# Optimization experiments

Hardware: AMD Instinct MI355X
Metric: run time of the kernel (lower is better)

## Reference

```python
import jax, jax.numpy as jnp
import numpy as np

B, S, T, D = 32, 8, 128, 768   # batch, num_sentences, seq_len, embedding_dim
A, L = 8, 8                    # num_args, arg_length


def _extract(sentence_embeddings, sentence_ids, token_ids):
    """Vectorized form of extract_embeddings_from_ids.

    For each (b, s, a): average, over nonzero token ids l, the embedding at the
    sentence position whose id equals token_ids[b,s,a,l]. token_id == 0 is skipped.
    sentence_ids are unique per sentence, so each id matches exactly one position
    (the only case where the original loop yields shape [B,S,A,D]).
    """
    valid = token_ids != 0                                            # [B,S,A,L]
    # match[b,s,a,l,t] = token matches sentence position t (and token is nonzero)
    match = (token_ids[..., None] == sentence_ids[:, :, None, None, :]) & valid[..., None]
    # gather matched embeddings per token: [B,S,A,L,D]
    gathered = jnp.einsum('bsalt,bstd->bsald', match.astype(sentence_embeddings.dtype),
                          sentence_embeddings)
    n_valid = jnp.maximum(valid.sum(-1), 1).astype(sentence_embeddings.dtype)  # [B,S,A]
    return gathered.sum(axis=3) / n_valid[..., None]                  # [B,S,A,D]


def setup_inputs() -> dict:
    key = jax.random.key(0)
    k_emb, k_p, k_a0, k_a1 = jax.random.split(key, 4)
    sentence_embeddings = jax.random.normal(k_emb, (B, S, T, D), dtype=jnp.float32)
    # unique token ids 1..T per sentence (0 is reserved as padding/skip)
    sentence_ids = jnp.broadcast_to(jnp.arange(1, T + 1, dtype=jnp.int64), (B, S, T))
    predicate_ids = jax.random.randint(k_p, (B, S, A, L), 0, T, dtype=jnp.int64)
    arg0_ids = jax.random.randint(k_a0, (B, S, A, L), 0, T, dtype=jnp.int64)
    arg1_ids = jax.random.randint(k_a1, (B, S, A, L), 0, T, dtype=jnp.int64)
    return {
        'sentence_embeddings': sentence_embeddings,
        'sentence_ids': sentence_ids,
        'predicate_ids': predicate_ids,
        'arg0_ids': arg0_ids,
        'arg1_ids': arg1_ids,
    }


def reference(sentence_embeddings, sentence_ids, predicate_ids, arg0_ids, arg1_ids):
    sentence_average_embeddings = sentence_embeddings.mean(axis=2)     # [B,S,D]
    predicate_embeddings = _extract(sentence_embeddings, sentence_ids, predicate_ids)
    arg0_embeddings = _extract(sentence_embeddings, sentence_ids, arg0_ids)
    arg1_embeddings = _extract(sentence_embeddings, sentence_ids, arg1_ids)
    return (sentence_average_embeddings, predicate_embeddings,
            arg0_embeddings, arg1_embeddings)
```

## Files before the change

### kernel.cpp

```cpp
#include <hip/hip_runtime.h>

namespace {
constexpr int B_ = 32, S_ = 8, T_ = 128, D_ = 768, A_ = 8, L_ = 8;
constexpr int BS = B_ * S_;
constexpr int MEAN_ELEMS = BS * D_;
constexpr int EXT_ELEMS  = BS * A_ * D_;
constexpr int MEAN_BLOCKS = BS * (D_ / 2) / 256;
constexpr int EXT_BLOCKS  = 3 * BS * A_;

__global__ void __launch_bounds__(256) srl_kernel(
    const float* __restrict__ emb,
    const int* __restrict__ sids,
    const int* __restrict__ pred,
    const int* __restrict__ arg0,
    const int* __restrict__ arg1,
    float* __restrict__ out)
{
    const int blk = blockIdx.x;
    const int tid = threadIdx.x;

    if (blk < MEAN_BLOCKS) {
        int idx = blk * 256 + tid;
        int d2  = idx % (D_ / 2);
        int bs  = idx / (D_ / 2);
        const float2* p = reinterpret_cast<const float2*>(emb)
                          + (size_t)bs * T_ * (D_ / 2) + d2;
        float sx = 0.f, sy = 0.f;
        #pragma unroll 8
        for (int t = 0; t < T_; ++t) {
            float2 v = p[(size_t)t * (D_ / 2)];
            sx += v.x; sy += v.y;
        }
        float2 r; r.x = sx * (1.0f / T_); r.y = sy * (1.0f / T_);
        reinterpret_cast<float2*>(out)[(size_t)bs * (D_ / 2) + d2] = r;
        return;
    }

    int eblk = blk - MEAN_BLOCKS;
    int e    = eblk / (BS * A_);
    int rem  = eblk % (BS * A_);
    int bs   = rem / A_;
    int a    = rem % A_;
    const int* tokp = (e == 0 ? pred : (e == 1 ? arg0 : arg1))
                      + (size_t)(bs * A_ + a) * L_;

    __shared__ int toks[L_];
    __shared__ int pos[L_];
    if (tid < L_) { toks[tid] = tokp[tid]; pos[tid] = -1; }
    __syncthreads();
    if (tid < T_) {
        int id = sids[(size_t)bs * T_ + tid];
        #pragma unroll
        for (int l = 0; l < L_; ++l)
            if (toks[l] != 0 && id == toks[l]) pos[l] = tid;
    }
    __syncthreads();

    int n = 0;
    #pragma unroll
    for (int l = 0; l < L_; ++l) n += (toks[l] != 0);
    float inv = 1.0f / (float)(n < 1 ? 1 : n);

    const float* base = emb + (size_t)bs * T_ * D_;
    float a0 = 0.f, a1 = 0.f, a2 = 0.f;
    #pragma unroll
    for (int l = 0; l < L_; ++l) {
        int p = pos[l];
        if (p >= 0) {
            const float* row = base + (size_t)p * D_;
            a0 += row[tid];
            a1 += row[tid + 256];
            a2 += row[tid + 512];
        }
    }
    float* o = out + MEAN_ELEMS + (size_t)e * EXT_ELEMS + (size_t)(bs * A_ + a) * D_;
    o[tid]       = a0 * inv;
    o[tid + 256] = a1 * inv;
    o[tid + 512] = a2 * inv;
}
}

extern "C" void kernel_launch(void* const* d_in, const int* in_sizes, int n_in,
                              void* d_out, int out_size, void* d_ws, size_t ws_size,
                              hipStream_t stream) {
    const float* emb  = (const float*)d_in[0];
    const int*   sids = (const int*)d_in[1];
    const int*   pred = (const int*)d_in[2];
    const int*   arg0 = (const int*)d_in[3];
    const int*   arg1 = (const int*)d_in[4];
    float* out = (float*)d_out;

    dim3 grid(MEAN_BLOCKS + EXT_BLOCKS);
    srl_kernel<<<grid, 256, 0, stream>>>(emb, sids, pred, arg0, arg1, out);
}
```

Baseline: 41.77 us.

## Fuse mean and gather into one block per sentence with per-token count weights

Replaces the separate mean blocks and per-(extraction,arg) gather blocks with a single block per sentence. Each block streams the sentence embeddings once, accumulating the mean and all 24 extraction outputs using packed per-position match counts held in shared memory, with double-buffered register loads. This avoids re-reading embedding rows across many small blocks, but it launches only 256 blocks of 384 threads, which lowers parallelism, and it raises register pressure from 24 float2 accumulators.

Measured after the change: 58.53 us. +40.1%, slower.

```diff
diff --git a/kernel.cpp b/kernel.cpp
--- a/kernel.cpp
+++ b/kernel.cpp
@@ -5,10 +5,11 @@
 constexpr int BS = B_ * S_;
 constexpr int MEAN_ELEMS = BS * D_;
 constexpr int EXT_ELEMS  = BS * A_ * D_;
-constexpr int MEAN_BLOCKS = BS * (D_ / 2) / 256;
-constexpr int EXT_BLOCKS  = 3 * BS * A_;
+constexpr int NO   = 3 * A_;
+constexpr int NTOK = NO * L_;
+constexpr int NTHR = 384;
 
-__global__ void __launch_bounds__(256) srl_kernel(
+__global__ void __launch_bounds__(NTHR, 1) srl_fused(
     const float* __restrict__ emb,
     const int* __restrict__ sids,
     const int* __restrict__ pred,
@@ -16,67 +17,107 @@
     const int* __restrict__ arg1,
     float* __restrict__ out)
 {
-    const int blk = blockIdx.x;
+    const int bs  = blockIdx.x;
     const int tid = threadIdx.x;
 
-    if (blk < MEAN_BLOCKS) {
-        int idx = blk * 256 + tid;
-        int d2  = idx % (D_ / 2);
-        int bs  = idx / (D_ / 2);
-        const float2* p = reinterpret_cast<const float2*>(emb)
-                          + (size_t)bs * T_ * (D_ / 2) + d2;
-        float sx = 0.f, sy = 0.f;
-        #pragma unroll 8
-        for (int t = 0; t < T_; ++t) {
-            float2 v = p[(size_t)t * (D_ / 2)];
-            sx += v.x; sy += v.y;
-        }
-        float2 r; r.x = sx * (1.0f / T_); r.y = sy * (1.0f / T_);
-        reinterpret_cast<float2*>(out)[(size_t)bs * (D_ / 2) + d2] = r;
-        return;
+    __shared__ int toks[NTOK];
+    __shared__ unsigned cnt[NO][T_];
+    __shared__ __attribute__((aligned(16))) unsigned packed[T_][8];
+    __shared__ float invs[NO];
+
+    if (tid < NTOK) {
+        int e = tid >> 6;
+        const int* p = (e == 0) ? pred : ((e == 1) ? arg0 : arg1);
+        toks[tid] = p[(size_t)bs * 64 + (tid & 63)];
     }
+    for (int i = tid; i < NO * T_; i += NTHR) ((unsigned*)cnt)[i] = 0u;
+    __syncthreads();
 
-    int eblk = blk - MEAN_BLOCKS;
-    int e    = eblk / (BS * A_);
-    int rem  = eblk % (BS * A_);
-    int bs   = rem / A_;
-    int a    = rem % A_;
-    const int* tokp = (e == 0 ? pred : (e == 1 ? arg0 : arg1))
-                      + (size_t)(bs * A_ + a) * L_;
-
-    __shared__ int toks[L_];
-    __shared__ int pos[L_];
-    if (tid < L_) { toks[tid] = tokp[tid]; pos[tid] = -1; }
-    __syncthreads();
     if (tid < T_) {
         int id = sids[(size_t)bs * T_ + tid];
+        if (id != 0) {
+            for (int i = 0; i < NTOK; ++i)
+                if (toks[i] == id) atomicAdd(&cnt[i >> 3][tid], 1u);
+        }
+    } else if (tid >= 320 && tid < 320 + NO) {
+        int o = tid - 320, n = 0;
         #pragma unroll
-        for (int l = 0; l < L_; ++l)
-            if (toks[l] != 0 && id == toks[l]) pos[l] = tid;
+        for (int l = 0; l < L_; ++l) n += (toks[o * L_ + l] != 0);
+        invs[o] = 1.0f / (float)(n < 1 ? 1 : n);
     }
     __syncthreads();
 
-    int n = 0;
+    if (tid < T_) {
+        #pragma unroll
+        for (int j = 0; j < 6; ++j) {
+            unsigned v = 0;
+            #pragma unroll
+            for (int k = 0; k < 4; ++k) v |= (cnt[j * 4 + k][tid] & 255u) << (8 * k);
+            packed[tid][j] = v;
+        }
+        packed[tid][6] = 0u;
+        packed[tid][7] = 0u;
+    }
+    __syncthreads();
+
+    const float2* eb = reinterpret_cast<const float2*>(emb + (size_t)bs * T_ * D_);
+    float2 accm = {0.f, 0.f};
+    float2 acc[NO];
     #pragma unroll
-    for (int l = 0; l < L_; ++l) n += (toks[l] != 0);
-    float inv = 1.0f / (float)(n < 1 ? 1 : n);
+    for (int o = 0; o < NO; ++o) acc[o] = {0.f, 0.f};
 
-    const float* base = emb + (size_t)bs * T_ * D_;
-    float a0 = 0.f, a1 = 0.f, a2 = 0.f;
+    float2 Abuf[8], Bbuf[8];
     #pragma unroll
-    for (int l = 0; l < L_; ++l) {
-        int p = pos[l];
-        if (p >= 0) {
-            const float* row = base + (size_t)p * D_;
-            a0 += row[tid];
-            a1 += row[tid + 256];
-            a2 += row[tid + 512];
+    for (int k = 0; k < 8; ++k) Abuf[k] = eb[(size_t)k * (D_ / 2) + tid];
+
+    auto proc = [&](const float2* buf, int tbase) {
+        #pragma unroll
+        for (int k = 0; k < 8; ++k) {
+            int t = tbase + k;
+            float2 v = buf[k];
+            accm.x += v.x; accm.y += v.y;
+            uint4 w0 = *reinterpret_cast<const uint4*>(&packed[t][0]);
+            uint2 w1 = *reinterpret_cast<const uint2*>(&packed[t][4]);
+            unsigned ws[6] = {w0.x, w0.y, w0.z, w0.w, w1.x, w1.y};
+            #pragma unroll
+            for (int j = 0; j < 6; ++j) {
+                unsigned wj = __builtin_amdgcn_readfirstlane(ws[j]);
+                if (wj) {
+                    #pragma unroll
+                    for (int kb = 0; kb < 4; ++kb) {
+                        unsigned c = (wj >> (8 * kb)) & 255u;
+                        if (c) {
+                            float fc = (float)c;
+                            acc[j * 4 + kb].x += fc * v.x;
+                            acc[j * 4 + kb].y += fc * v.y;
+                        }
+                    }
+                }
+            }
         }
+    };
+
+    for (int t0 = 0; t0 < T_; t0 += 16) {
+        #pragma unroll
+        for (int k = 0; k < 8; ++k) Bbuf[k] = eb[(size_t)(t0 + 8 + k) * (D_ / 2) + tid];
+        proc(Abuf, t0);
+        if (t0 + 16 < T_) {
+            #pragma unroll
+            for (int k = 0; k < 8; ++k) Abuf[k] = eb[(size_t)(t0 + 16 + k) * (D_ / 2) + tid];
+        }
+        proc(Bbuf, t0 + 8);
     }
-    float* o = out + MEAN_ELEMS + (size_t)e * EXT_ELEMS + (size_t)(bs * A_ + a) * D_;
-    o[tid]       = a0 * inv;
-    o[tid + 256] = a1 * inv;
-    o[tid + 512] = a2 * inv;
+
+    reinterpret_cast<float2*>(out)[(size_t)bs * (D_ / 2) + tid] =
+        {accm.x * (1.0f / T_), accm.y * (1.0f / T_)};
+    #pragma unroll
+    for (int o = 0; o < NO; ++o) {
+        int e = o >> 3, a = o & 7;
+        float iv = invs[o];
+        float2* po = reinterpret_cast<float2*>(
+            out + MEAN_ELEMS + (size_t)e * EXT_ELEMS + (size_t)(bs * A_ + a) * D_);
+        po[tid] = {acc[o].x * iv, acc[o].y * iv};
+    }
 }
 }
 
@@ -90,6 +131,5 @@
     const int*   arg1 = (const int*)d_in[4];
     float* out = (float*)d_out;
 
-    dim3 grid(MEAN_BLOCKS + EXT_BLOCKS);
-    srl_kernel<<<grid, 256, 0, stream>>>(emb, sids, pred, arg0, arg1, out);
+    srl_fused<<<dim3(BS), dim3(NTHR), 0, stream>>>(emb, sids, pred, arg0, arg1, out);
 }
```

## Split mean into T-chunked partial kernel and fuse three extractions per block

Applied to the files above, without the earlier changes.

Replaces the single fused kernel with two launches. The first computes float4 partial sums of the sentence mean over four T-chunks into workspace. The second reduces those partials and handles all three extractions (predicate, arg0, arg1) for one (bs, a) in a single block, sharing the id-matching pass and the embedding-row loads across the three. A fallback path without workspace runs a full-T mean kernel instead. This adds a second launch and a workspace round trip, and the mean kernels use only 192 threads per block.

Result: slower. 45.65 us (+9.3%).

```diff
diff --git a/kernel.cpp b/kernel.cpp
--- a/kernel.cpp
+++ b/kernel.cpp
@@ -5,78 +5,124 @@
 constexpr int BS = B_ * S_;
 constexpr int MEAN_ELEMS = BS * D_;
 constexpr int EXT_ELEMS  = BS * A_ * D_;
-constexpr int MEAN_BLOCKS = BS * (D_ / 2) / 256;
-constexpr int EXT_BLOCKS  = 3 * BS * A_;
+constexpr int TSPLIT = 4, TCH = T_ / TSPLIT;
+constexpr int D4 = D_ / 4;
+constexpr int RED_BLOCKS = BS * D4 / 256;
+constexpr int EXT_BLOCKS = BS * A_;
+constexpr size_t WS_FLOATS = (size_t)TSPLIT * BS * D_;
 
-__global__ void __launch_bounds__(256) srl_kernel(
+__global__ void __launch_bounds__(192) k_mean_partial(
+    const float* __restrict__ emb, float* __restrict__ ws)
+{
+    int blk = blockIdx.x;
+    int bs = blk >> 2, ch = blk & 3;
+    int tid = threadIdx.x;
+    const float4* p = reinterpret_cast<const float4*>(emb + (size_t)bs * T_ * D_)
+                      + (size_t)(ch * TCH) * D4 + tid;
+    float4 acc = {0.f, 0.f, 0.f, 0.f};
+    #pragma unroll 8
+    for (int t = 0; t < TCH; ++t) {
+        float4 v = p[(size_t)t * D4];
+        acc.x += v.x; acc.y += v.y; acc.z += v.z; acc.w += v.w;
+    }
+    reinterpret_cast<float4*>(ws)[(size_t)(ch * BS + bs) * D4 + tid] = acc;
+}
+
+__global__ void __launch_bounds__(192) k_mean_full(
+    const float* __restrict__ emb, float* __restrict__ out)
+{
+    int bs = blockIdx.x, tid = threadIdx.x;
+    const float4* p = reinterpret_cast<const float4*>(emb + (size_t)bs * T_ * D_) + tid;
+    float4 acc = {0.f, 0.f, 0.f, 0.f};
+    #pragma unroll 8
+    for (int t = 0; t < T_; ++t) {
+        float4 v = p[(size_t)t * D4];
+        acc.x += v.x; acc.y += v.y; acc.z += v.z; acc.w += v.w;
+    }
+    const float s = 1.0f / T_;
+    float4 r = {acc.x * s, acc.y * s, acc.z * s, acc.w * s};
+    reinterpret_cast<float4*>(out)[(size_t)bs * D4 + tid] = r;
+}
+
+template <bool WITH_RED>
+__global__ void __launch_bounds__(256) k_tail(
     const float* __restrict__ emb,
     const int* __restrict__ sids,
     const int* __restrict__ pred,
     const int* __restrict__ arg0,
     const int* __restrict__ arg1,
+    const float* __restrict__ ws,
     float* __restrict__ out)
 {
-    const int blk = blockIdx.x;
-    const int tid = threadIdx.x;
+    int blk = blockIdx.x;
+    int tid = threadIdx.x;
 
-    if (blk < MEAN_BLOCKS) {
-        int idx = blk * 256 + tid;
-        int d2  = idx % (D_ / 2);
-        int bs  = idx / (D_ / 2);
-        const float2* p = reinterpret_cast<const float2*>(emb)
-                          + (size_t)bs * T_ * (D_ / 2) + d2;
-        float sx = 0.f, sy = 0.f;
-        #pragma unroll 8
-        for (int t = 0; t < T_; ++t) {
-            float2 v = p[(size_t)t * (D_ / 2)];
-            sx += v.x; sy += v.y;
+    if (WITH_RED) {
+        if (blk < RED_BLOCKS) {
+            int idx = blk * 256 + tid;
+            const float4* w = reinterpret_cast<const float4*>(ws);
+            float4 a = w[idx];
+            float4 b = w[(size_t)BS * D4 + idx];
+            float4 c = w[2 * (size_t)BS * D4 + idx];
+            float4 d = w[3 * (size_t)BS * D4 + idx];
+            const float s = 1.0f / T_;
+            float4 r = {(a.x + b.x + c.x + d.x) * s, (a.y + b.y + c.y + d.y) * s,
+                        (a.z + b.z + c.z + d.z) * s, (a.w + b.w + c.w + d.w) * s};
+            reinterpret_cast<float4*>(out)[idx] = r;
+            return;
         }
-        float2 r; r.x = sx * (1.0f / T_); r.y = sy * (1.0f / T_);
-        reinterpret_cast<float2*>(out)[(size_t)bs * (D_ / 2) + d2] = r;
-        return;
+        blk -= RED_BLOCKS;
     }
 
-    int eblk = blk - MEAN_BLOCKS;
-    int e    = eblk / (BS * A_);
-    int rem  = eblk % (BS * A_);
-    int bs   = rem / A_;
-    int a    = rem % A_;
-    const int* tokp = (e == 0 ? pred : (e == 1 ? arg0 : arg1))
-                      + (size_t)(bs * A_ + a) * L_;
+    int bs = blk >> 3, a = blk & 7;
+    constexpr int NT = 3 * L_;
+    __shared__ int toks[NT];
+    __shared__ int pos[NT];
+    __shared__ float invs[3];
 
-    __shared__ int toks[L_];
-    __shared__ int pos[L_];
-    if (tid < L_) { toks[tid] = tokp[tid]; pos[tid] = -1; }
+    if (tid < NT) {
+        int e = tid >> 3, l = tid & 7;
+        const int* p = (e == 0) ? pred : ((e == 1) ? arg0 : arg1);
+        toks[tid] = p[(size_t)(bs * A_ + a) * L_ + l];
+        pos[tid] = -1;
+    }
     __syncthreads();
     if (tid < T_) {
         int id = sids[(size_t)bs * T_ + tid];
         #pragma unroll
-        for (int l = 0; l < L_; ++l)
-            if (toks[l] != 0 && id == toks[l]) pos[l] = tid;
+        for (int i = 0; i < NT; ++i)
+            if (toks[i] != 0 && toks[i] == id) pos[i] = tid;
+    } else if (tid >= 128 && tid < 128 + 3) {
+        int e = tid - 128, n = 0;
+        #pragma unroll
+        for (int l = 0; l < L_; ++l) n += (toks[e * L_ + l] != 0);
+        invs[e] = 1.0f / (float)(n < 1 ? 1 : n);
     }
     __syncthreads();
 
-    int n = 0;
+    const float* base = emb + (size_t)bs * T_ * D_;
+    float acc[3][3] = {};
     #pragma unroll
-    for (int l = 0; l < L_; ++l) n += (toks[l] != 0);
-    float inv = 1.0f / (float)(n < 1 ? 1 : n);
-
-    const float* base = emb + (size_t)bs * T_ * D_;
-    float a0 = 0.f, a1 = 0.f, a2 = 0.f;
-    #pragma unroll
-    for (int l = 0; l < L_; ++l) {
-        int p = pos[l];
-        if (p >= 0) {
-            const float* row = base + (size_t)p * D_;
-            a0 += row[tid];
-            a1 += row[tid + 256];
-            a2 += row[tid + 512];
+    for (int e = 0; e < 3; ++e) {
+        #pragma unroll
+        for (int l = 0; l < L_; ++l) {
+            int p = pos[e * L_ + l];
+            if (p >= 0) {
+                const float* row = base + (size_t)p * D_;
+                acc[e][0] += row[tid];
+                acc[e][1] += row[tid + 256];
+                acc[e][2] += row[tid + 512];
+            }
         }
     }
-    float* o = out + MEAN_ELEMS + (size_t)e * EXT_ELEMS + (size_t)(bs * A_ + a) * D_;
-    o[tid]       = a0 * inv;
-    o[tid + 256] = a1 * inv;
-    o[tid + 512] = a2 * inv;
+    #pragma unroll
+    for (int e = 0; e < 3; ++e) {
+        float iv = invs[e];
+        float* o = out + MEAN_ELEMS + (size_t)e * EXT_ELEMS + (size_t)(bs * A_ + a) * D_;
+        o[tid]       = acc[e][0] * iv;
+        o[tid + 256] = acc[e][1] * iv;
+        o[tid + 512] = acc[e][2] * iv;
+    }
 }
 }
 
@@ -89,7 +135,15 @@
     const int*   arg0 = (const int*)d_in[3];
     const int*   arg1 = (const int*)d_in[4];
     float* out = (float*)d_out;
+    float* ws  = (float*)d_ws;
 
-    dim3 grid(MEAN_BLOCKS + EXT_BLOCKS);
-    srl_kernel<<<grid, 256, 0, stream>>>(emb, sids, pred, arg0, arg1, out);
+    if (ws_size >= WS_FLOATS * sizeof(float)) {
+        k_mean_partial<<<dim3(BS * TSPLIT), dim3(192), 0, stream>>>(emb, ws);
+        k_tail<true><<<dim3(RED_BLOCKS + EXT_BLOCKS), dim3(256), 0, stream>>>(
+            emb, sids, pred, arg0, arg1, ws, out);
+    } else {
+        k_mean_full<<<dim3(BS), dim3(192), 0, stream>>>(emb, out);
+        k_tail<false><<<dim3(EXT_BLOCKS), dim3(256), 0, stream>>>(
+            emb, sids, pred, arg0, arg1, ws, out);
+    }
 }
```
